# Kernel optimization log

Hardware: AMD Instinct MI355X
Metric: run time of the kernel (lower is better)

The kernel has to match this reference:

```python
import jax, jax.numpy as jnp
import numpy as np

B, R, M, L, H = 256, 2048, 65536, 64, 4  # batch, reservoir, memory_size, key_len, read_heads


def setup_inputs() -> dict:
    key = jax.random.key(0)
    ks = jax.random.split(key, 4)
    s = 1.0 / np.sqrt(R).astype(np.float32)  # ~xavier scale for Linear weights
    return {
        "reservoir_state": jax.random.normal(ks[0], (B, R), dtype=jnp.float32),
        "memory": jax.random.normal(ks[1], (1, M, L), dtype=jnp.float32),
        "Wk": jax.random.normal(ks[2], (H * L, R), dtype=jnp.float32) * s,
        "bk": jnp.zeros((H * L,), dtype=jnp.float32),
        "Wb": jax.random.normal(ks[3], (H, R), dtype=jnp.float32) * s,
        "bb": jnp.zeros((H,), dtype=jnp.float32),
    }


def reference(reservoir_state, memory, Wk, bk, Wb, bb):
    b = reservoir_state.shape[0]
    h = Wb.shape[0]
    # key projection -> [B, H, L]
    keys = (reservoir_state @ Wk.T + bk).reshape(b, h, -1)
    # per-head key strength, relu-gated -> [B, H]
    betas = jax.nn.relu(reservoir_state @ Wb.T + bb)
    # content addressing: dot(keys, memory rows) -> [B, H, M]
    dots = jnp.einsum('bhl,ml->bhm', keys, memory[0])
    # normalize by key norm (as in original: sqrt(sum(keys^2)))
    dots = dots / jnp.sqrt(jnp.sum(keys ** 2, axis=-1, keepdims=True))
    # beta-scaled softmax over memory slots
    return jax.nn.softmax(betas[:, :, None] * dots, axis=-1)
```

## Files before the change

kernel.cpp:

```cpp
#include <hip/hip_runtime.h>
#include <hip/hip_bf16.h>

#define BB   256
#define RR   2048
#define MM   65536
#define LL   64
#define HH   4
#define NROW 1024
#define KEYS 256

typedef float f32x4 __attribute__((ext_vector_type(4)));
typedef short short8 __attribute__((ext_vector_type(8)));

#define MFMA(A,B,C) __builtin_amdgcn_mfma_f32_16x16x32_bf16((A),(B),(C),0,0,0)
#define LOG2E 1.4426950408889634f
#define EXP2F(x) __builtin_amdgcn_exp2f(x)

__device__ __forceinline__ unsigned short bf16_rn(float x) {
    union { float f; unsigned int u; } v; v.f = x;
    unsigned int r = v.u + 0x7FFFu + ((v.u >> 16) & 1u);
    return (unsigned short)(r >> 16);
}
__device__ __forceinline__ float bf16_to_f(unsigned short h) {
    union { float f; unsigned int u; } v; v.u = ((unsigned int)h) << 16; return v.f;
}
__device__ __forceinline__ void split8_store(const float* x, unsigned short* hi, unsigned short* lo) {
    unsigned int ph[4], pl[4];
#pragma unroll
    for (int j = 0; j < 4; ++j) {
        unsigned short h0 = bf16_rn(x[2*j]),   l0 = bf16_rn(x[2*j]   - bf16_to_f(h0));
        unsigned short h1 = bf16_rn(x[2*j+1]), l1 = bf16_rn(x[2*j+1] - bf16_to_f(h1));
        ph[j] = (unsigned int)h0 | ((unsigned int)h1 << 16);
        pl[j] = (unsigned int)l0 | ((unsigned int)l1 << 16);
    }
    ((uint4*)hi)[0] = make_uint4(ph[0], ph[1], ph[2], ph[3]);
    ((uint4*)lo)[0] = make_uint4(pl[0], pl[1], pl[2], pl[3]);
}

__global__ __launch_bounds__(256) void transpose_k(const float* __restrict__ in,
                                                   float* __restrict__ out,
                                                   int NR, int NC) {
    __shared__ float t[64 * 65];
    int r0 = blockIdx.x * 64, c0 = blockIdx.y * 64;
    int lane = threadIdx.x & 63, w = threadIdx.x >> 6;
#pragma unroll
    for (int i = 0; i < 16; ++i) {
        int rr = i * 4 + w;
        t[lane * 65 + rr] = in[(size_t)(r0 + rr) * NC + c0 + lane];
    }
    __syncthreads();
#pragma unroll
    for (int i = 0; i < 16; ++i) {
        int cc = i * 4 + w;
        out[(size_t)(c0 + cc) * NR + r0 + lane] = t[cc * 65 + lane];
    }
}

__global__ __launch_bounds__(256) void prep_mem(const float* __restrict__ mem,
                                                unsigned short* __restrict__ bhi,
                                                unsigned short* __restrict__ blo,
                                                float* __restrict__ normpart) {
    __shared__ float t[128 * 68];
    __shared__ float rowsq[128];
    int blk = blockIdx.x, tid = threadIdx.x;
    const f32x4* src = (const f32x4*)(mem + (size_t)blk * 128 * LL);
#pragma unroll
    for (int i = 0; i < 8; ++i) {
        int idx = i * 256 + tid;
        int row = idx >> 4, c4 = idx & 15;
        *(f32x4*)&t[row * 68 + c4 * 4] = src[idx];
    }
    __syncthreads();
    if (tid < 128) {
        const float* rp = t + tid * 68;
        float s = 0.f;
#pragma unroll
        for (int k = 0; k < 64; ++k) s = fmaf(rp[k], rp[k], s);
        rowsq[tid] = s;
    }
    __syncthreads();
    if (tid < 64) {
        float m = fmaxf(rowsq[tid], rowsq[tid + 64]);
#pragma unroll
        for (int off = 1; off < 64; off <<= 1) m = fmaxf(m, __shfl_xor(m, off, 64));
        if (tid == 0) normpart[blk] = m;
    }
#pragma unroll
    for (int i = 0; i < 4; ++i) {
        int slot = i * 256 + tid;
        int lane = slot & 63, frag_l = slot >> 6;
        int t_l = frag_l >> 1, c = frag_l & 1;
        int row = t_l * 16 + (lane & 15);
        int k0 = c * 32 + (lane >> 4) * 8;
        const float* p = t + row * 68 + k0;
        float x[8];
#pragma unroll
        for (int j = 0; j < 8; ++j) x[j] = p[j];
        size_t gslot = ((size_t)blk * 16 + frag_l) * 64 + lane;
        split8_store(x, bhi + gslot * 8, blo + gslot * 8);
    }
}

__global__ __launch_bounds__(256) void k0_keys(const float* __restrict__ S,
                                               const float* __restrict__ WkT,
                                               float* __restrict__ kpart) {
    __shared__ float sl[8 * 256];
    int bg = blockIdx.x, kc = blockIdx.y, tid = threadIdx.x;
    int b0 = bg * 8;
#pragma unroll
    for (int bi = 0; bi < 8; ++bi)
        sl[bi * 256 + tid] = S[(size_t)(b0 + bi) * RR + kc * 256 + tid];
    __syncthreads();
    float acc[8] = {0,0,0,0,0,0,0,0};
    const float* wp = WkT + (size_t)kc * 256 * KEYS + tid;
#pragma unroll 4
    for (int kk = 0; kk < 256; ++kk) {
        float wv = wp[kk * KEYS];
#pragma unroll
        for (int bi = 0; bi < 8; ++bi)
            acc[bi] = fmaf(sl[bi * 256 + kk], wv, acc[bi]);
    }
    float* op = kpart + (size_t)kc * BB * KEYS + (size_t)b0 * KEYS + tid;
#pragma unroll
    for (int bi = 0; bi < 8; ++bi)
        op[bi * KEYS] = acc[bi];
}

__global__ __launch_bounds__(256) void k1_finalize(const float* __restrict__ S,
                                                   const float* __restrict__ kpart,
                                                   const float* __restrict__ bk,
                                                   const float* __restrict__ Wb,
                                                   const float* __restrict__ bb,
                                                   const float* __restrict__ normpart,
                                                   float* __restrict__ q_rm,
                                                   float* __restrict__ brow) {
    int bh = blockIdx.x, b = bh >> 2, h = bh & 3;
    int tid = threadIdx.x, lane = tid & 63, w = tid >> 6;
    float p = 0.f;
#pragma unroll
    for (int i = 0; i < 8; ++i) {
        int k = i * 256 + tid;
        p += S[(size_t)b * RR + k] * Wb[(size_t)h * RR + k];
    }
    float nm = fmaxf(normpart[tid], normpart[256 + tid]);
#pragma unroll
    for (int off = 1; off < 64; off <<= 1) {
        p  += __shfl_xor(p, off, 64);
        nm  = fmaxf(nm, __shfl_xor(nm, off, 64));
    }
    __shared__ float red[4], redm[4];
    if (lane == 0) { red[w] = p; redm[w] = nm; }
    __syncthreads();
    if (tid < 64) {
        float beta = red[0] + red[1] + red[2] + red[3] + bb[h];
        beta = fmaxf(beta, 0.f);
        float maxn = sqrtf(fmaxf(fmaxf(redm[0], redm[1]), fmaxf(redm[2], redm[3])));
        float kv = bk[h * LL + lane];
#pragma unroll
        for (int c = 0; c < 8; ++c)
            kv += kpart[(size_t)c * BB * KEYS + (size_t)b * KEYS + h * LL + lane];
        float sq = kv * kv;
#pragma unroll
        for (int off = 1; off < 64; off <<= 1) sq += __shfl_xor(sq, off, 64);
        float scale = beta * LOG2E / sqrtf(sq);
        q_rm[(size_t)bh * LL + lane] = kv * scale;
        if (lane == 0) brow[bh] = beta * maxn * LOG2E;
    }
}

__global__ __launch_bounds__(256) void prep_a(const float* __restrict__ q_rm,
                                              unsigned short* __restrict__ ahi,
                                              unsigned short* __restrict__ alo) {
    int gid = blockIdx.x * 256 + threadIdx.x;
    int lane = gid & 63, frag = gid >> 6;
    int rtg = frag >> 1, c = frag & 1;
    int row = rtg * 16 + (lane & 15);
    int k0 = c * 32 + (lane >> 4) * 8;
    const float4* src = (const float4*)(q_rm + (size_t)row * LL + k0);
    float4 x0 = src[0], x1 = src[1];
    float x[8] = {x0.x, x0.y, x0.z, x0.w, x1.x, x1.y, x1.z, x1.w};
    split8_store(x, ahi + (size_t)gid * 8, alo + (size_t)gid * 8);
}

__device__ __forceinline__ void decode_wg(int bx, int& mblk, int& rg) {
    int wg = ((bx & 7) << 7) | (bx >> 3);
    mblk = wg >> 4; rg = wg & 15;
}

__global__ __launch_bounds__(256) void k2_mfma(const unsigned short* __restrict__ bhi,
                                               const unsigned short* __restrict__ blo,
                                               const unsigned short* __restrict__ ahi,
                                               const unsigned short* __restrict__ alo,
                                               const float* __restrict__ brow,
                                               float* __restrict__ psum) {
    int mblk, rg; decode_wg(blockIdx.x, mblk, rg);
    int tid = threadIdx.x, w = tid >> 6, lane = tid & 63;
    int g = lane >> 4;
    short8 Ah[4][2], Al[4][2];
#pragma unroll
    for (int rt = 0; rt < 4; ++rt)
#pragma unroll
        for (int c = 0; c < 2; ++c) {
            size_t off = ((size_t)((rg * 4 + rt) * 2 + c) * 64 + lane) * 8;
            Ah[rt][c] = *(const short8*)(ahi + off);
            Al[rt][c] = *(const short8*)(alo + off);
        }
    float br[4][4];
#pragma unroll
    for (int rt = 0; rt < 4; ++rt)
#pragma unroll
        for (int r = 0; r < 4; ++r)
            br[rt][r] = brow[rg * 64 + rt * 16 + g * 4 + r];
    float s[4][4] = {{0.f}};
    int t0 = mblk * 64 + w * 16;
    short8 Bh0, Bh1, Bl0, Bl1;
    {
        size_t o = (size_t)t0 * 1024 + (size_t)lane * 8;
        Bh0 = *(const short8*)(bhi + o); Bh1 = *(const short8*)(bhi + o + 512);
        Bl0 = *(const short8*)(blo + o); Bl1 = *(const short8*)(blo + o + 512);
    }
#pragma unroll 4
    for (int ti = 0; ti < 16; ++ti) {
        int tn = t0 + ((ti < 15) ? ti + 1 : 15);
        size_t on = (size_t)tn * 1024 + (size_t)lane * 8;
        short8 nh0 = *(const short8*)(bhi + on);
        short8 nh1 = *(const short8*)(bhi + on + 512);
        short8 nl0 = *(const short8*)(blo + on);
        short8 nl1 = *(const short8*)(blo + on + 512);
#pragma unroll
        for (int rt = 0; rt < 4; ++rt) {
            f32x4 C = {0.f, 0.f, 0.f, 0.f};
            C = MFMA(Ah[rt][0], Bh0, C);
            C = MFMA(Ah[rt][1], Bh1, C);
            C = MFMA(Al[rt][0], Bh0, C);
            C = MFMA(Al[rt][1], Bh1, C);
            C = MFMA(Ah[rt][0], Bl0, C);
            C = MFMA(Ah[rt][1], Bl1, C);
#pragma unroll
            for (int r = 0; r < 4; ++r)
                s[rt][r] += EXP2F(C[r] - br[rt][r]);
        }
        Bh0 = nh0; Bh1 = nh1; Bl0 = nl0; Bl1 = nl1;
    }
#pragma unroll
    for (int rt = 0; rt < 4; ++rt)
#pragma unroll
        for (int r = 0; r < 4; ++r) {
            float v = s[rt][r];
            v += __shfl_xor(v, 1, 64);
            v += __shfl_xor(v, 2, 64);
            v += __shfl_xor(v, 4, 64);
            v += __shfl_xor(v, 8, 64);
            s[rt][r] = v;
        }
    if ((lane & 15) == 0) {
        int col = mblk * 4 + w;
#pragma unroll
        for (int rt = 0; rt < 4; ++rt)
#pragma unroll
            for (int r = 0; r < 4; ++r) {
                int row = rg * 64 + rt * 16 + g * 4 + r;
                psum[(size_t)row * 256 + col] = s[rt][r];
            }
    }
}

__global__ __launch_bounds__(256) void k3_combine(const float* __restrict__ psum,
                                                  float* __restrict__ ginv) {
    int row = blockIdx.x, tid = threadIdx.x, lane = tid & 63, w = tid >> 6;
    float v = psum[(size_t)row * 256 + tid];
#pragma unroll
    for (int off = 1; off < 64; off <<= 1) v += __shfl_xor(v, off, 64);
    __shared__ float sm[4];
    if (lane == 0) sm[w] = v;
    __syncthreads();
    if (tid == 0) ginv[row] = 1.0f / (sm[0] + sm[1] + sm[2] + sm[3]);
}

__global__ __launch_bounds__(256) void k4_mfma(const unsigned short* __restrict__ bhi,
                                               const unsigned short* __restrict__ blo,
                                               const unsigned short* __restrict__ ahi,
                                               const unsigned short* __restrict__ alo,
                                               const float* __restrict__ brow,
                                               const float* __restrict__ ginv,
                                               float* __restrict__ out) {
    __shared__ float ot[4][64 * 20];
    int mblk, rg; decode_wg(blockIdx.x, mblk, rg);
    int tid = threadIdx.x, w = tid >> 6, lane = tid & 63;
    int g = lane >> 4;
    float* wt = &ot[w][0];
    short8 Ah[4][2], Al[4][2];
#pragma unroll
    for (int rt = 0; rt < 4; ++rt)
#pragma unroll
        for (int c = 0; c < 2; ++c) {
            size_t off = ((size_t)((rg * 4 + rt) * 2 + c) * 64 + lane) * 8;
            Ah[rt][c] = *(const short8*)(ahi + off);
            Al[rt][c] = *(const short8*)(alo + off);
        }
    float br[4][4], gv[4][4];
#pragma unroll
    for (int rt = 0; rt < 4; ++rt)
#pragma unroll
        for (int r = 0; r < 4; ++r) {
            int row = rg * 64 + rt * 16 + g * 4 + r;
            br[rt][r] = brow[row];
            gv[rt][r] = ginv[row];
        }
    int t0 = mblk * 64 + w * 16;
    short8 Bh0, Bh1, Bl0, Bl1;
    {
        size_t o = (size_t)t0 * 1024 + (size_t)lane * 8;
        Bh0 = *(const short8*)(bhi + o); Bh1 = *(const short8*)(bhi + o + 512);
        Bl0 = *(const short8*)(blo + o); Bl1 = *(const short8*)(blo + o + 512);
    }
#pragma unroll 2
    for (int ti = 0; ti < 16; ++ti) {
        int t = t0 + ti;
        int tn = t0 + ((ti < 15) ? ti + 1 : 15);
        size_t on = (size_t)tn * 1024 + (size_t)lane * 8;
        short8 nh0 = *(const short8*)(bhi + on);
        short8 nh1 = *(const short8*)(bhi + on + 512);
        short8 nl0 = *(const short8*)(blo + on);
        short8 nl1 = *(const short8*)(blo + on + 512);
#pragma unroll
        for (int rt = 0; rt < 4; ++rt) {
            f32x4 C = {0.f, 0.f, 0.f, 0.f};
            C = MFMA(Ah[rt][0], Bh0, C);
            C = MFMA(Ah[rt][1], Bh1, C);
            C = MFMA(Al[rt][0], Bh0, C);
            C = MFMA(Al[rt][1], Bh1, C);
            C = MFMA(Ah[rt][0], Bl0, C);
            C = MFMA(Ah[rt][1], Bl1, C);
#pragma unroll
            for (int r = 0; r < 4; ++r)
                wt[(rt * 16 + g * 4 + r) * 20 + (lane & 15)] =
                    EXP2F(C[r] - br[rt][r]) * gv[rt][r];
        }
#pragma unroll
        for (int j = 0; j < 4; ++j) {
            int rl = j * 16 + (lane >> 2);
            f32x4 v = *(const f32x4*)&wt[rl * 20 + (lane & 3) * 4];
            float* dst = out + (size_t)(rg * 64 + rl) * MM + (size_t)t * 16 + (lane & 3) * 4;
            __builtin_nontemporal_store(v, (f32x4*)dst);
        }
        Bh0 = nh0; Bh1 = nh1; Bl0 = nl0; Bl1 = nl1;
    }
}

extern "C" void kernel_launch(void* const* d_in, const int* in_sizes, int n_in,
                              void* d_out, int out_size, void* d_ws, size_t ws_size,
                              hipStream_t stream) {
    const float* S   = (const float*)d_in[0];
    const float* mem = (const float*)d_in[1];
    const float* Wk  = (const float*)d_in[2];
    const float* bk  = (const float*)d_in[3];
    const float* Wb  = (const float*)d_in[4];
    const float* bb  = (const float*)d_in[5];
    float* out = (float*)d_out;

    float* WkT      = (float*)d_ws;
    float* kpart    = WkT   + (size_t)RR * KEYS;
    float* q_rm     = kpart + (size_t)8 * BB * KEYS;
    float* psum     = q_rm  + (size_t)NROW * LL;
    float* brow     = psum  + (size_t)NROW * 256;
    float* ginv     = brow  + NROW;
    float* normpart = ginv  + NROW;
    unsigned short* bhi = (unsigned short*)(normpart + 512);
    unsigned short* blo = bhi + (size_t)8192 * 512;
    unsigned short* ahi = blo + (size_t)8192 * 512;
    unsigned short* alo = ahi + (size_t)128 * 512;

    transpose_k<<<dim3(BB / 64, RR / 64), 256, 0, stream>>>(Wk, WkT, KEYS, RR);
    prep_mem   <<<512,         256, 0, stream>>>(mem, bhi, blo, normpart);
    k0_keys    <<<dim3(32, 8), 256, 0, stream>>>(S, WkT, kpart);
    k1_finalize<<<NROW,        256, 0, stream>>>(S, kpart, bk, Wb, bb, normpart, q_rm, brow);
    prep_a     <<<32,          256, 0, stream>>>(q_rm, ahi, alo);
    k2_mfma    <<<1024,        256, 0, stream>>>(bhi, blo, ahi, alo, brow, psum);
    k3_combine <<<NROW,        256, 0, stream>>>(psum, ginv);
    k4_mfma    <<<1024,        256, 0, stream>>>(bhi, blo, ahi, alo, brow, ginv, out);
}
```

Baseline: 395.6 us.

## Retile output kernel to 16 rows by 4096 columns with block-wide coalesced stores

The final MFMA/softmax-write kernel now gives each workgroup 16 output rows and 4096 columns instead of 64 rows and 1024 columns. Results are staged in a shared LDS buffer and written as 2KB contiguous row segments with nontemporal stores, replacing the old 64-byte fragments. It also adds an XCD-style block index swizzle. In exchange, each B tile is reused across one row tile instead of four, which raises B reads, and two __syncthreads per chunk are added.

```diff
diff --git a/kernel.cpp b/kernel.cpp
--- a/kernel.cpp
+++ b/kernel.cpp
@@ -284,67 +284,68 @@
                                                const float* __restrict__ brow,
                                                const float* __restrict__ ginv,
                                                float* __restrict__ out) {
-    __shared__ float ot[4][64 * 20];
-    int mblk, rg; decode_wg(blockIdx.x, mblk, rg);
+    __shared__ float ot[16 * 516];
+    int bx = blockIdx.x;
+    int wg = ((bx & 7) << 7) | (bx >> 3);
+    int mblk = wg >> 6, rg = wg & 63;
     int tid = threadIdx.x, w = tid >> 6, lane = tid & 63;
     int g = lane >> 4;
-    float* wt = &ot[w][0];
-    short8 Ah[4][2], Al[4][2];
-#pragma unroll
-    for (int rt = 0; rt < 4; ++rt)
-#pragma unroll
-        for (int c = 0; c < 2; ++c) {
-            size_t off = ((size_t)((rg * 4 + rt) * 2 + c) * 64 + lane) * 8;
-            Ah[rt][c] = *(const short8*)(ahi + off);
-            Al[rt][c] = *(const short8*)(alo + off);
-        }
-    float br[4][4], gv[4][4];
-#pragma unroll
-    for (int rt = 0; rt < 4; ++rt)
-#pragma unroll
-        for (int r = 0; r < 4; ++r) {
-            int row = rg * 64 + rt * 16 + g * 4 + r;
-            br[rt][r] = brow[row];
-            gv[rt][r] = ginv[row];
-        }
-    int t0 = mblk * 64 + w * 16;
+    short8 Ah[2], Al[2];
+#pragma unroll
+    for (int c = 0; c < 2; ++c) {
+        size_t off = ((size_t)(rg * 2 + c) * 64 + lane) * 8;
+        Ah[c] = *(const short8*)(ahi + off);
+        Al[c] = *(const short8*)(alo + off);
+    }
+    float br[4], gv[4];
+#pragma unroll
+    for (int r = 0; r < 4; ++r) {
+        int row = rg * 16 + g * 4 + r;
+        br[r] = brow[row];
+        gv[r] = ginv[row];
+    }
+    int tbase = mblk * 256 + w * 8;
     short8 Bh0, Bh1, Bl0, Bl1;
     {
-        size_t o = (size_t)t0 * 1024 + (size_t)lane * 8;
+        size_t o = (size_t)tbase * 1024 + (size_t)lane * 8;
         Bh0 = *(const short8*)(bhi + o); Bh1 = *(const short8*)(bhi + o + 512);
         Bl0 = *(const short8*)(blo + o); Bl1 = *(const short8*)(blo + o + 512);
     }
-#pragma unroll 2
-    for (int ti = 0; ti < 16; ++ti) {
-        int t = t0 + ti;
-        int tn = t0 + ((ti < 15) ? ti + 1 : 15);
-        size_t on = (size_t)tn * 1024 + (size_t)lane * 8;
-        short8 nh0 = *(const short8*)(bhi + on);
-        short8 nh1 = *(const short8*)(bhi + on + 512);
-        short8 nl0 = *(const short8*)(blo + on);
-        short8 nl1 = *(const short8*)(blo + on + 512);
-#pragma unroll
-        for (int rt = 0; rt < 4; ++rt) {
+    for (int c = 0; c < 8; ++c) {
+#pragma unroll
+        for (int k = 0; k < 8; ++k) {
+            int j = c * 8 + k;
+            int jn = (j < 63) ? j + 1 : 63;
+            int tn = tbase + (jn >> 3) * 32 + (jn & 7);
+            size_t on = (size_t)tn * 1024 + (size_t)lane * 8;
+            short8 nh0 = *(const short8*)(bhi + on);
+            short8 nh1 = *(const short8*)(bhi + on + 512);
+            short8 nl0 = *(const short8*)(blo + on);
+            short8 nl1 = *(const short8*)(blo + on + 512);
             f32x4 C = {0.f, 0.f, 0.f, 0.f};
-            C = MFMA(Ah[rt][0], Bh0, C);
-            C = MFMA(Ah[rt][1], Bh1, C);
-            C = MFMA(Al[rt][0], Bh0, C);
-            C = MFMA(Al[rt][1], Bh1, C);
-            C = MFMA(Ah[rt][0], Bl0, C);
-            C = MFMA(Ah[rt][1], Bl1, C);
+            C = MFMA(Ah[0], Bh0, C);
+            C = MFMA(Ah[1], Bh1, C);
+            C = MFMA(Al[0], Bh0, C);
+            C = MFMA(Al[1], Bh1, C);
+            C = MFMA(Ah[0], Bl0, C);
+            C = MFMA(Ah[1], Bl1, C);
+            int cbase = w * 128 + k * 16 + (lane & 15);
 #pragma unroll
             for (int r = 0; r < 4; ++r)
-                wt[(rt * 16 + g * 4 + r) * 20 + (lane & 15)] =
-                    EXP2F(C[r] - br[rt][r]) * gv[rt][r];
-        }
-#pragma unroll
-        for (int j = 0; j < 4; ++j) {
-            int rl = j * 16 + (lane >> 2);
-            f32x4 v = *(const f32x4*)&wt[rl * 20 + (lane & 3) * 4];
-            float* dst = out + (size_t)(rg * 64 + rl) * MM + (size_t)t * 16 + (lane & 3) * 4;
+                ot[(g * 4 + r) * 516 + cbase] = EXP2F(C[r] - br[r]) * gv[r];
+            Bh0 = nh0; Bh1 = nh1; Bl0 = nl0; Bl1 = nl1;
+        }
+        __syncthreads();
+        size_t gbase = (size_t)mblk * 4096 + (size_t)c * 512;
+#pragma unroll
+        for (int i = 0; i < 8; ++i) {
+            int flat = i * 256 + tid;
+            int rl = flat >> 7, slot = flat & 127;
+            f32x4 v = *(const f32x4*)&ot[rl * 516 + slot * 4];
+            float* dst = out + (size_t)(rg * 16 + rl) * MM + gbase + (size_t)slot * 4;
             __builtin_nontemporal_store(v, (f32x4*)dst);
         }
-        Bh0 = nh0; Bh1 = nh1; Bl0 = nl0; Bl1 = nl1;
+        __syncthreads();
     }
 }
 
```

After: 355.4 us. 1.11x faster.
